# Optimization experiments

Hardware: AMD Instinct MI355X
Metric: run time of the kernel (lower is better)

The kernel has to match this reference:

```python
import jax, jax.numpy as jnp
import numpy as np

N_NODES = 100000
N_EDGES = 3200000
NFEAT = 128
NHID = 128
NCLASS = 8
BN_EPS = 1e-5


def setup_inputs() -> dict:
    key = jax.random.key(0)
    ks = jax.random.split(key, 8)
    x = jax.random.normal(ks[0], (N_NODES, NFEAT), dtype=jnp.float32)
    edge_index = jax.random.randint(ks[1], (2, N_EDGES), 0, N_NODES, dtype=jnp.int64)
    # GCNConv params: weight [nfeat, nhid] (glorot), bias [nhid]
    lim = float(np.sqrt(6.0 / (NFEAT + NHID)))
    W = jax.random.uniform(ks[2], (NFEAT, NHID), minval=-lim, maxval=lim, dtype=jnp.float32)
    b_gc = jnp.zeros((NHID,), dtype=jnp.float32)
    # BatchNorm1d params
    gamma = jnp.ones((NHID,), dtype=jnp.float32)
    beta = jnp.zeros((NHID,), dtype=jnp.float32)
    # fc head: (nhid/2) -> nclass, xavier_uniform, zero bias
    lim2 = float(np.sqrt(6.0 / (NHID // 2 + NCLASS)))
    fc_w = jax.random.uniform(ks[3], (NCLASS, NHID // 2), minval=-lim2, maxval=lim2, dtype=jnp.float32)
    fc_b = jnp.zeros((NCLASS,), dtype=jnp.float32)
    return {"x": x, "edge_index": edge_index, "W": W, "b_gc": b_gc,
            "gamma": gamma, "beta": beta, "fc_w": fc_w, "fc_b": fc_b}


def _gcn_conv(x, edge_index, W, b):
    """PyG GCNConv: add self-loops, symmetric norm, linear, gather-scatter, bias."""
    N = x.shape[0]
    loops = jnp.arange(N, dtype=edge_index.dtype)
    src = jnp.concatenate([edge_index[0], loops])  # source (row / x_j)
    dst = jnp.concatenate([edge_index[1], loops])  # target (col / aggregation index)
    # degree of target nodes (edge weight = 1)
    deg = jax.ops.segment_sum(jnp.ones_like(dst, dtype=x.dtype), dst, num_segments=N)
    dinv = jnp.where(deg > 0, jax.lax.rsqrt(deg), 0.0)
    norm = dinv[src] * dinv[dst]  # [E+N]
    h = x @ W  # [N, nhid]
    msg = h[src] * norm[:, None]  # gather + scale
    out = jax.ops.segment_sum(msg, dst, num_segments=N)  # scatter-add
    return out + b


def _batchnorm(h, gamma, beta):
    mean = jnp.mean(h, axis=0)
    var = jnp.mean(jnp.square(h - mean), axis=0)  # biased, training-mode
    return gamma * (h - mean) * jax.lax.rsqrt(var + BN_EPS) + beta


def reference(x, edge_index, W, b_gc, gamma, beta, fc_w, fc_b):
    h = _gcn_conv(x, edge_index, W, b_gc)
    embed = _batchnorm(h, gamma, beta)
    half = embed.shape[1] // 2
    out = embed[:, :half] @ fc_w.T + fc_b
    return (out, embed)
```

## Files before the change

### kernel.cpp

```cpp
#include <hip/hip_runtime.h>
#include <hip/hip_bf16.h>
#include <math.h>

#define N_NODES 100000
#define N_EDGES 3200000
#define NFEAT 128
#define NHID 128
#define NCLASS 8
#define BN_EPS 1e-5f
#define CB 512
#define NBC 196
#define EPB 8192
#define PART_BLOCKS 391
#define WT_BLOCKS 64

typedef __attribute__((ext_vector_type(8))) short short8;
typedef __attribute__((ext_vector_type(4))) float f32x4;

__device__ __forceinline__ short f2bf(float f) {
    __hip_bfloat16 b = __float2bfloat16(f);
    return *reinterpret_cast<short*>(&b);
}
__device__ __forceinline__ float bf_lo(unsigned u) { return __uint_as_float(u << 16); }
__device__ __forceinline__ float bf_hi(unsigned u) { return __uint_as_float(u & 0xffff0000u); }


__global__ __launch_bounds__(256) void k_chist(const int* __restrict__ dst,
                                               int* __restrict__ ghist,
                                               const float* __restrict__ W,
                                               unsigned short* __restrict__ Wt,
                                               uint4* __restrict__ hbz) {
    if (blockIdx.x >= PART_BLOCKS) {
        int idx = (blockIdx.x - PART_BLOCKS) * 256 + threadIdx.x;
        if (idx < 16) hbz[idx] = (uint4){0u, 0u, 0u, 0u};
        int k = idx >> 7, n = idx & 127;
        Wt[n * NFEAT + k] = (unsigned short)f2bf(W[idx]);
        return;
    }
    __shared__ int lh[NBC];
    const int tid = threadIdx.x;
    if (tid < NBC) lh[tid] = 0;
    __syncthreads();
    const int4* dst4 = (const int4*)dst;
    const int q0 = blockIdx.x * (EPB / 4) + tid;
#pragma unroll
    for (int i = 0; i < 8; ++i) {
        int q = q0 + i * 256;
        if (q < N_EDGES / 4) {
            int4 d = dst4[q];
            atomicAdd(&lh[d.x >> 9], 1);
            atomicAdd(&lh[d.y >> 9], 1);
            atomicAdd(&lh[d.z >> 9], 1);
            atomicAdd(&lh[d.w >> 9], 1);
        }
    }
    __syncthreads();
    if (tid < NBC) {
        int c = lh[tid];
        if (c) atomicAdd(&ghist[tid], c);
    }
}

__global__ __launch_bounds__(512) void k_cscan(const int* __restrict__ ghist,
                                               int* __restrict__ coff,
                                               int* __restrict__ ccur,
                                               int* __restrict__ off,
                                               float* __restrict__ stats,
                                               int* __restrict__ ticket) {
    __shared__ int tmp[512];
    const int t = threadIdx.x;
    if (t < 256) stats[t] = 0.f;
    if (t == 0) *ticket = 0;
    int v = (t < NBC) ? ghist[t] : 0;
    tmp[t] = v;
    __syncthreads();
    for (int d = 1; d < 512; d <<= 1) {
        int u = (t >= d) ? tmp[t - d] : 0;
        __syncthreads();
        tmp[t] += u;
        __syncthreads();
    }
    int excl = tmp[t] - v;
    if (t < NBC) {
        coff[t] = excl;
        ccur[t] = excl;
    }
    if (t == NBC - 1) {
        coff[NBC] = tmp[t];
        off[N_NODES] = tmp[t];
    }
}


__global__ __launch_bounds__(256) void k_part(const int* __restrict__ src,
                                              const int* __restrict__ dst,
                                              int* __restrict__ ccur,
                                              unsigned* __restrict__ epack) {
    __shared__ int lh[NBC];
    __shared__ int lstart[NBC];
    __shared__ int adj[NBC];
    __shared__ int stmp[256];
    __shared__ unsigned sorted[EPB];
    __shared__ unsigned short bkt[EPB];
    const int tid = threadIdx.x;
    if (tid < NBC) lh[tid] = 0;
    __syncthreads();
    const int4* src4 = (const int4*)src;
    const int4* dst4 = (const int4*)dst;
    const int q0 = blockIdx.x * (EPB / 4) + tid;
    int4 sv[8], dv[8];
    int rk[32];
#pragma unroll
    for (int i = 0; i < 8; ++i) {
        int q = q0 + i * 256;
        if (q < N_EDGES / 4) {
            sv[i] = src4[q];
            dv[i] = dst4[q];
            rk[i * 4 + 0] = atomicAdd(&lh[dv[i].x >> 9], 1);
            rk[i * 4 + 1] = atomicAdd(&lh[dv[i].y >> 9], 1);
            rk[i * 4 + 2] = atomicAdd(&lh[dv[i].z >> 9], 1);
            rk[i * 4 + 3] = atomicAdd(&lh[dv[i].w >> 9], 1);
        } else dv[i].x = -1;
    }
    __syncthreads();
    int v = (tid < NBC) ? lh[tid] : 0;
    stmp[tid] = v;
    __syncthreads();
    for (int d = 1; d < 256; d <<= 1) {
        int u = (tid >= d) ? stmp[tid - d] : 0;
        __syncthreads();
        stmp[tid] += u;
        __syncthreads();
    }
    if (tid < NBC) {
        int ls = stmp[tid] - v;
        lstart[tid] = ls;
        adj[tid] = (v ? atomicAdd(&ccur[tid], v) : 0) - ls;
    }
    __syncthreads();
#pragma unroll
    for (int i = 0; i < 8; ++i) {
        if (dv[i].x >= 0) {
            int b, p;
            b = dv[i].x >> 9; p = lstart[b] + rk[i * 4 + 0];
            sorted[p] = ((unsigned)sv[i].x << 9) | (unsigned)(dv[i].x & 511); bkt[p] = (unsigned short)b;
            b = dv[i].y >> 9; p = lstart[b] + rk[i * 4 + 1];
            sorted[p] = ((unsigned)sv[i].y << 9) | (unsigned)(dv[i].y & 511); bkt[p] = (unsigned short)b;
            b = dv[i].z >> 9; p = lstart[b] + rk[i * 4 + 2];
            sorted[p] = ((unsigned)sv[i].z << 9) | (unsigned)(dv[i].z & 511); bkt[p] = (unsigned short)b;
            b = dv[i].w >> 9; p = lstart[b] + rk[i * 4 + 3];
            sorted[p] = ((unsigned)sv[i].w << 9) | (unsigned)(dv[i].w & 511); bkt[p] = (unsigned short)b;
        }
    }
    __syncthreads();
    const int vcnt = stmp[255];
    for (int p = tid; p < vcnt; p += 256)
        epack[p + adj[bkt[p]]] = sorted[p];
}


__global__ __launch_bounds__(256) void k_fine(const unsigned* __restrict__ epack,
                                              const int* __restrict__ coff,
                                              int* __restrict__ off,
                                              float* __restrict__ dinv,
                                              int* __restrict__ esrc) {
    __shared__ int lh[CB], lcur[CB], lsc[256];
    const int tid = threadIdx.x;
    const int b = blockIdx.x;
    const int node0 = b << 9;
    lh[tid] = 0;
    lh[tid + 256] = 0;
    __syncthreads();
    const int lo = coff[b], hiEnd = coff[b + 1];
    for (int i = lo + tid; i < hiEnd; i += 256)
        atomicAdd(&lh[epack[i] & 511u], 1);
    __syncthreads();
    int v0 = lh[2 * tid], v1 = lh[2 * tid + 1];
    int s = v0 + v1;
    lsc[tid] = s;
    __syncthreads();
    for (int d = 1; d < 256; d <<= 1) {
        int u = (tid >= d) ? lsc[tid - d] : 0;
        __syncthreads();
        lsc[tid] += u;
        __syncthreads();
    }
    int pairExcl = lsc[tid] - s;
    lcur[2 * tid] = pairExcl;
    lcur[2 * tid + 1] = pairExcl + v0;
    int n0 = node0 + 2 * tid, n1 = n0 + 1;
    if (n0 < N_NODES) { off[n0] = lo + pairExcl;      dinv[n0] = rsqrtf((float)(v0 + 1)); }
    if (n1 < N_NODES) { off[n1] = lo + pairExcl + v0; dinv[n1] = rsqrtf((float)(v1 + 1)); }
    __syncthreads();
    for (int i = lo + tid; i < hiEnd; i += 256) {
        unsigned p = epack[i];
        int pos = atomicAdd(&lcur[p & 511u], 1);
        esrc[lo + pos] = (int)(p >> 9);
    }
}


#define WSTRIDE 136
#define XSTRIDE 136
__global__ __launch_bounds__(256) void k_gemm(const float* __restrict__ x,
                                              const unsigned short* __restrict__ Wt,
                                              const float* __restrict__ dinv,
                                              unsigned short* __restrict__ hb) {
    __shared__ __align__(16) short wlds[NHID * WSTRIDE];
    __shared__ __align__(16) short xl[64 * XSTRIDE];
    const int tid = threadIdx.x;
    const int row0 = blockIdx.x * 64;

    const unsigned* Wt32 = (const unsigned*)Wt;
    unsigned* wl32 = (unsigned*)wlds;
#pragma unroll
    for (int i = 0; i < 32; ++i) {
        int d = tid + i * 256;
        int n = d >> 6, kp = d & 63;
        wl32[n * (WSTRIDE / 2) + kp] = Wt32[d];
    }
    const float4* x4 = (const float4*)x;
#pragma unroll
    for (int i = 0; i < 8; ++i) {
        int idx = tid + i * 256;
        int r = idx >> 5, c4 = idx & 31;
        int gr = row0 + r;
        float4 vv = (gr < N_NODES) ? x4[(size_t)gr * 32 + c4]
                                   : (float4){0.f, 0.f, 0.f, 0.f};
        short4 t;
        t.x = f2bf(vv.x); t.y = f2bf(vv.y); t.z = f2bf(vv.z); t.w = f2bf(vv.w);
        *(short4*)&xl[r * XSTRIDE + c4 * 4] = t;
    }
    __syncthreads();

    const int wid = tid >> 6, lane = tid & 63;
    const int qw = lane >> 4, lr = lane & 15;

    short8 a[4];
#pragma unroll
    for (int ks = 0; ks < 4; ++ks)
        a[ks] = *(const short8*)&xl[(wid * 16 + lr) * XSTRIDE + ks * 32 + qw * 8];

    f32x4 acc[8];
#pragma unroll
    for (int nt = 0; nt < 8; ++nt) acc[nt] = (f32x4){0.f, 0.f, 0.f, 0.f};

#pragma unroll
    for (int nt = 0; nt < 8; ++nt) {
#pragma unroll
        for (int ks = 0; ks < 4; ++ks) {
            short8 bfr = *(const short8*)&wlds[(nt * 16 + lr) * WSTRIDE + ks * 32 + qw * 8];
            acc[nt] = __builtin_amdgcn_mfma_f32_16x16x32_bf16(a[ks], bfr, acc[nt], 0, 0, 0);
        }
    }

    const int rbase = blockIdx.x * 64 + wid * 16 + qw * 4;
    float dv[4];
#pragma unroll
    for (int j = 0; j < 4; ++j) dv[j] = (rbase + j < N_NODES) ? dinv[rbase + j] : 0.f;
#pragma unroll
    for (int j = 0; j < 4; ++j) {
        int r = rbase + j;
        if (r >= N_NODES) continue;
#pragma unroll
        for (int nt = 0; nt < 8; ++nt)
            hb[(size_t)r * NHID + nt * 16 + lr] = (unsigned short)f2bf(dv[j] * acc[nt][j]);
    }
}


__global__ __launch_bounds__(256) void k_agg(const int* __restrict__ off,
                                             const int* __restrict__ esrc,
                                             const float* __restrict__ dinv,
                                             const uint2* __restrict__ hbq,
                                             float4* __restrict__ agg4) {
    const int node = (blockIdx.x << 2) | (threadIdx.x >> 6);
    const int lane = threadIdx.x & 63;
    const int hl = lane >> 5;
    const int cl = lane & 31;
    if (node >= N_NODES) return;

    const float dn = dinv[node];
    const int self = hl ? N_NODES : node;
    uint2 u0 = hbq[(size_t)self * 32 + cl];
    float aAx = bf_lo(u0.x), aAy = bf_hi(u0.x), aAz = bf_lo(u0.y), aAw = bf_hi(u0.y);
    float aBx = 0.f, aBy = 0.f, aBz = 0.f, aBw = 0.f;
    float aCx = 0.f, aCy = 0.f, aCz = 0.f, aCw = 0.f;
    float aDx = 0.f, aDy = 0.f, aDz = 0.f, aDw = 0.f;

    const int begin = off[node], end = off[node + 1];
    for (int base = begin; base < end; base += 64) {
        int m = end - base;
        if (m > 64) m = 64;
        int sv = (lane < m) ? esrc[base + lane] : N_NODES;
        const int kmax = (m + 7) >> 3;
        for (int k = 0; k < kmax; ++k) {
            int sA = __shfl(sv, 8 * k + 0 + hl);
            int sB = __shfl(sv, 8 * k + 2 + hl);
            int sC = __shfl(sv, 8 * k + 4 + hl);
            int sD = __shfl(sv, 8 * k + 6 + hl);
            uint2 uA = hbq[(size_t)sA * 32 + cl];
            uint2 uB = hbq[(size_t)sB * 32 + cl];
            uint2 uC = hbq[(size_t)sC * 32 + cl];
            uint2 uD = hbq[(size_t)sD * 32 + cl];
            aAx += bf_lo(uA.x); aAy += bf_hi(uA.x); aAz += bf_lo(uA.y); aAw += bf_hi(uA.y);
            aBx += bf_lo(uB.x); aBy += bf_hi(uB.x); aBz += bf_lo(uB.y); aBw += bf_hi(uB.y);
            aCx += bf_lo(uC.x); aCy += bf_hi(uC.x); aCz += bf_lo(uC.y); aCw += bf_hi(uC.y);
            aDx += bf_lo(uD.x); aDy += bf_hi(uD.x); aDz += bf_lo(uD.y); aDw += bf_hi(uD.y);
        }
    }
    float ax = (aAx + aBx) + (aCx + aDx);
    float ay = (aAy + aBy) + (aCy + aDy);
    float az = (aAz + aBz) + (aCz + aDz);
    float aw = (aAw + aBw) + (aCw + aDw);
    ax += __shfl_xor(ax, 32);
    ay += __shfl_xor(ay, 32);
    az += __shfl_xor(az, 32);
    aw += __shfl_xor(aw, 32);
    if (hl == 0) {
        float4 o;
        o.x = ax * dn; o.y = ay * dn; o.z = az * dn; o.w = aw * dn;
        agg4[(size_t)node * 32 + cl] = o;
    }
}


__global__ __launch_bounds__(256) void k_stats(const float* __restrict__ agg,
                                               float* __restrict__ stats,
                                               int* __restrict__ ticket,
                                               const float* __restrict__ gamma,
                                               const float* __restrict__ beta,
                                               float* __restrict__ ss) {
    const int cb = threadIdx.x & 31;
    const int rg = threadIdx.x >> 5;
    const float4* a4 = (const float4*)agg;
    float4 s = {0.f, 0.f, 0.f, 0.f}, s2 = {0.f, 0.f, 0.f, 0.f};
    for (int r = blockIdx.x * 8 + rg; r < N_NODES; r += gridDim.x * 8) {
        float4 v = a4[(size_t)r * 32 + cb];
        s.x += v.x; s.y += v.y; s.z += v.z; s.w += v.w;
        s2.x += v.x * v.x; s2.y += v.y * v.y; s2.z += v.z * v.z; s2.w += v.w * v.w;
    }
    __shared__ float4 ls[256], ls2[256];
    __shared__ int lastflag;
    ls[threadIdx.x] = s;
    ls2[threadIdx.x] = s2;
    __syncthreads();
    if (rg == 0) {
        float4 ts = ls[cb], t2 = ls2[cb];
#pragma unroll
        for (int g = 1; g < 8; ++g) {
            float4 v = ls[g * 32 + cb], w = ls2[g * 32 + cb];
            ts.x += v.x; ts.y += v.y; ts.z += v.z; ts.w += v.w;
            t2.x += w.x; t2.y += w.y; t2.z += w.z; t2.w += w.w;
        }
        atomicAdd(&stats[cb * 4 + 0], ts.x);
        atomicAdd(&stats[cb * 4 + 1], ts.y);
        atomicAdd(&stats[cb * 4 + 2], ts.z);
        atomicAdd(&stats[cb * 4 + 3], ts.w);
        atomicAdd(&stats[128 + cb * 4 + 0], t2.x);
        atomicAdd(&stats[128 + cb * 4 + 1], t2.y);
        atomicAdd(&stats[128 + cb * 4 + 2], t2.z);
        atomicAdd(&stats[128 + cb * 4 + 3], t2.w);
    }
    __threadfence();
    __syncthreads();
    if (threadIdx.x == 0)
        lastflag = (atomicAdd(ticket, 1) == (int)gridDim.x - 1) ? 1 : 0;
    __syncthreads();
    if (lastflag && threadIdx.x < NHID) {
        int c = threadIdx.x;
        float sum = atomicAdd(&stats[c], 0.f);
        float sq  = atomicAdd(&stats[128 + c], 0.f);
        float mean = sum / (float)N_NODES;
        float var = fmaxf(sq / (float)N_NODES - mean * mean, 0.f);
        float inv = rsqrtf(var + BN_EPS);
        float sc = gamma[c] * inv;
        ss[c] = sc;
        ss[128 + c] = beta[c] - mean * sc;
    }
}


__global__ __launch_bounds__(256) void k_bnfc(float* __restrict__ embed,
                                              const float* __restrict__ ss,
                                              const float* __restrict__ fc_w,
                                              const float* __restrict__ fc_b,
                                              float* __restrict__ out) {
    __shared__ float se[64][68];
    __shared__ float sw[8][68];
    __shared__ float sb[8];
    const int tid = threadIdx.x;
    const int row0 = blockIdx.x * 64;
    {
        int d = tid;
        sw[d >> 6][d & 63] = fc_w[d];
        d = tid + 256;
        sw[d >> 6][d & 63] = fc_w[d];
        if (tid < 8) sb[tid] = fc_b[tid];
    }
    float4* ef4 = (float4*)embed;
    const float4* ssc4 = (const float4*)ss;
    const float4* ssh4 = (const float4*)(ss + 128);
#pragma unroll
    for (int i = 0; i < 8; ++i) {
        int d = tid + i * 256;
        int r = d >> 5;
        int cb = d & 31;
        int gr = row0 + r;
        if (gr < N_NODES) {
            float4 v = ef4[(size_t)gr * 32 + cb];
            float4 sc = ssc4[cb], sh = ssh4[cb];
            v.x = fmaf(v.x, sc.x, sh.x);
            v.y = fmaf(v.y, sc.y, sh.y);
            v.z = fmaf(v.z, sc.z, sh.z);
            v.w = fmaf(v.w, sc.w, sh.w);
            ef4[(size_t)gr * 32 + cb] = v;
            if (cb < 16) {
                se[r][cb * 4 + 0] = v.x; se[r][cb * 4 + 1] = v.y;
                se[r][cb * 4 + 2] = v.z; se[r][cb * 4 + 3] = v.w;
            }
        } else if (cb < 16) {
            se[r][cb * 4 + 0] = 0.f; se[r][cb * 4 + 1] = 0.f;
            se[r][cb * 4 + 2] = 0.f; se[r][cb * 4 + 3] = 0.f;
        }
    }
    __syncthreads();
    const int r = tid >> 2;
    const int j0 = (tid & 3) * 2;
    const int gr = row0 + r;
#pragma unroll
    for (int jj = 0; jj < 2; ++jj) {
        int j = j0 + jj;
        float s = sb[j];
#pragma unroll
        for (int k = 0; k < 64; ++k) s = fmaf(se[r][k], sw[j][k], s);
        if (gr < N_NODES) out[(size_t)gr * NCLASS + j] = s;
    }
}


extern "C" void kernel_launch(void* const* d_in, const int* in_sizes, int n_in,
                              void* d_out, int out_size, void* d_ws, size_t ws_size,
                              hipStream_t stream) {
    const float* x     = (const float*)d_in[0];
    const int*   ei    = (const int*)d_in[1];
    const float* W     = (const float*)d_in[2];
    const float* gamma = (const float*)d_in[4];
    const float* beta  = (const float*)d_in[5];
    const float* fc_w  = (const float*)d_in[6];
    const float* fc_b  = (const float*)d_in[7];

    const int* src = ei;
    const int* dst = ei + N_EDGES;

    float* out   = (float*)d_out;
    float* embed = (float*)d_out + (size_t)N_NODES * NCLASS;

    char* ws = (char*)d_ws;
    size_t o = 0;
    unsigned* epack = (unsigned*)(ws + o);          o += (size_t)N_EDGES * 4;
    unsigned short* hb = (unsigned short*)(ws + o); o += (size_t)(N_NODES + 1) * NHID * 2;
    o = (o + 255) & ~(size_t)255;
    int* esrc   = (int*)(ws + o);                   o += (size_t)N_EDGES * 4;
    int* off    = (int*)(ws + o);                   o += (size_t)(N_NODES + 1) * 4;
    float* dinv = (float*)(ws + o);                 o += (size_t)N_NODES * 4;
    unsigned short* Wt = (unsigned short*)(ws + o); o += (size_t)NFEAT * NHID * 2;
    float* stats = (float*)(ws + o);                o += 256 * 4;
    float* ss    = (float*)(ws + o);                o += 256 * 4;
    int* ghist   = (int*)(ws + o);                  o += NBC * 4;
    int* coff    = (int*)(ws + o);                  o += (NBC + 1) * 4;
    int* ccur    = (int*)(ws + o);                  o += NBC * 4;
    int* ticket  = (int*)(ws + o);                  o += 4;

    hipMemsetAsync(ghist, 0, NBC * 4, stream);

    k_chist<<<PART_BLOCKS + WT_BLOCKS, 256, 0, stream>>>(dst, ghist, W, Wt,
                                                         (uint4*)(hb + (size_t)N_NODES * NHID));
    k_cscan<<<1, 512, 0, stream>>>(ghist, coff, ccur, off, stats, ticket);
    k_part<<<PART_BLOCKS, 256, 0, stream>>>(src, dst, ccur, epack);
    k_fine<<<NBC, 256, 0, stream>>>(epack, coff, off, dinv, esrc);

    k_gemm<<<(N_NODES + 63) / 64, 256, 0, stream>>>(x, Wt, dinv, hb);

    k_agg<<<(N_NODES + 3) / 4, 256, 0, stream>>>(off, esrc, dinv, (const uint2*)hb, (float4*)embed);

    k_stats<<<512, 256, 0, stream>>>(embed, stats, ticket, gamma, beta, ss);

    k_bnfc<<<(N_NODES + 63) / 64, 256, 0, stream>>>(embed, ss, fc_w, fc_b, out);
}
```

Measured before the change: 319.7 us.

## Fuse BN stats and BN+FC into one kernel with a grid-wide flag barrier

Merges the stats and BN/FC kernels into one persistent 512-block kernel. The last block to finish the stats computes the scale and shift, then sets a flag that the other blocks spin on before running the BN+FC tiles. This saves a launch and may reuse cached embed data. The histogram now writes per-block partials instead of using a memset and global atomics, the W transpose moves into the single-block scan kernel, and the bucket array shrinks to bytes. The spin barrier is only safe if all 512 blocks are co-resident. The serial 391-iteration reduction and the 16K-element transpose in a single block may also add latency.

```diff
diff --git a/kernel.cpp b/kernel.cpp
--- a/kernel.cpp
+++ b/kernel.cpp
@@ -12,7 +12,8 @@
 #define NBC 196
 #define EPB 8192
 #define PART_BLOCKS 391
-#define WT_BLOCKS 64
+#define NT_BNFC 1563
+#define SB_BLOCKS 512
 
 typedef __attribute__((ext_vector_type(8))) short short8;
 typedef __attribute__((ext_vector_type(4))) float f32x4;
@@ -26,17 +27,7 @@
 
 
 __global__ __launch_bounds__(256) void k_chist(const int* __restrict__ dst,
-                                               int* __restrict__ ghist,
-                                               const float* __restrict__ W,
-                                               unsigned short* __restrict__ Wt,
-                                               uint4* __restrict__ hbz) {
-    if (blockIdx.x >= PART_BLOCKS) {
-        int idx = (blockIdx.x - PART_BLOCKS) * 256 + threadIdx.x;
-        if (idx < 16) hbz[idx] = (uint4){0u, 0u, 0u, 0u};
-        int k = idx >> 7, n = idx & 127;
-        Wt[n * NFEAT + k] = (unsigned short)f2bf(W[idx]);
-        return;
-    }
+                                               int* __restrict__ ghist2) {
     __shared__ int lh[NBC];
     const int tid = threadIdx.x;
     if (tid < NBC) lh[tid] = 0;
@@ -55,23 +46,34 @@
         }
     }
     __syncthreads();
-    if (tid < NBC) {
-        int c = lh[tid];
-        if (c) atomicAdd(&ghist[tid], c);
-    }
-}
-
-__global__ __launch_bounds__(512) void k_cscan(const int* __restrict__ ghist,
+    if (tid < NBC) ghist2[blockIdx.x * NBC + tid] = lh[tid];
+}
+
+
+__global__ __launch_bounds__(512) void k_cscan(const int* __restrict__ ghist2,
                                                int* __restrict__ coff,
                                                int* __restrict__ ccur,
                                                int* __restrict__ off,
                                                float* __restrict__ stats,
-                                               int* __restrict__ ticket) {
+                                               int* __restrict__ ticket,
+                                               int* __restrict__ flag,
+                                               const float* __restrict__ W,
+                                               unsigned short* __restrict__ Wt,
+                                               unsigned short* __restrict__ hbzrow) {
     __shared__ int tmp[512];
     const int t = threadIdx.x;
     if (t < 256) stats[t] = 0.f;
-    if (t == 0) *ticket = 0;
-    int v = (t < NBC) ? ghist[t] : 0;
+    if (t == 0) { *ticket = 0; *flag = 0; }
+    if (t < NHID) hbzrow[t] = 0;
+#pragma unroll
+    for (int i = 0; i < 32; ++i) {
+        int idx = t + i * 512;
+        int k = idx >> 7, n = idx & 127;
+        Wt[n * NFEAT + k] = (unsigned short)f2bf(W[idx]);
+    }
+    int v = 0;
+    if (t < NBC)
+        for (int b = 0; b < PART_BLOCKS; ++b) v += ghist2[b * NBC + t];
     tmp[t] = v;
     __syncthreads();
     for (int d = 1; d < 512; d <<= 1) {
@@ -101,7 +103,7 @@
     __shared__ int adj[NBC];
     __shared__ int stmp[256];
     __shared__ unsigned sorted[EPB];
-    __shared__ unsigned short bkt[EPB];
+    __shared__ unsigned char bkt[EPB];
     const int tid = threadIdx.x;
     if (tid < NBC) lh[tid] = 0;
     __syncthreads();
@@ -143,13 +145,13 @@
         if (dv[i].x >= 0) {
             int b, p;
             b = dv[i].x >> 9; p = lstart[b] + rk[i * 4 + 0];
-            sorted[p] = ((unsigned)sv[i].x << 9) | (unsigned)(dv[i].x & 511); bkt[p] = (unsigned short)b;
+            sorted[p] = ((unsigned)sv[i].x << 9) | (unsigned)(dv[i].x & 511); bkt[p] = (unsigned char)b;
             b = dv[i].y >> 9; p = lstart[b] + rk[i * 4 + 1];
-            sorted[p] = ((unsigned)sv[i].y << 9) | (unsigned)(dv[i].y & 511); bkt[p] = (unsigned short)b;
+            sorted[p] = ((unsigned)sv[i].y << 9) | (unsigned)(dv[i].y & 511); bkt[p] = (unsigned char)b;
             b = dv[i].z >> 9; p = lstart[b] + rk[i * 4 + 2];
-            sorted[p] = ((unsigned)sv[i].z << 9) | (unsigned)(dv[i].z & 511); bkt[p] = (unsigned short)b;
+            sorted[p] = ((unsigned)sv[i].z << 9) | (unsigned)(dv[i].z & 511); bkt[p] = (unsigned char)b;
             b = dv[i].w >> 9; p = lstart[b] + rk[i * 4 + 3];
-            sorted[p] = ((unsigned)sv[i].w << 9) | (unsigned)(dv[i].w & 511); bkt[p] = (unsigned short)b;
+            sorted[p] = ((unsigned)sv[i].w << 9) | (unsigned)(dv[i].w & 511); bkt[p] = (unsigned char)b;
         }
     }
     __syncthreads();
@@ -325,116 +327,129 @@
 }
 
 
-__global__ __launch_bounds__(256) void k_stats(const float* __restrict__ agg,
-                                               float* __restrict__ stats,
-                                               int* __restrict__ ticket,
-                                               const float* __restrict__ gamma,
-                                               const float* __restrict__ beta,
-                                               float* __restrict__ ss) {
-    const int cb = threadIdx.x & 31;
-    const int rg = threadIdx.x >> 5;
-    const float4* a4 = (const float4*)agg;
-    float4 s = {0.f, 0.f, 0.f, 0.f}, s2 = {0.f, 0.f, 0.f, 0.f};
-    for (int r = blockIdx.x * 8 + rg; r < N_NODES; r += gridDim.x * 8) {
-        float4 v = a4[(size_t)r * 32 + cb];
-        s.x += v.x; s.y += v.y; s.z += v.z; s.w += v.w;
-        s2.x += v.x * v.x; s2.y += v.y * v.y; s2.z += v.z * v.z; s2.w += v.w * v.w;
-    }
-    __shared__ float4 ls[256], ls2[256];
+__global__ __launch_bounds__(256) void k_statsbnfc(float* __restrict__ embed,
+                                                   float* __restrict__ stats,
+                                                   int* __restrict__ ticket,
+                                                   int* __restrict__ flag,
+                                                   const float* __restrict__ gamma,
+                                                   const float* __restrict__ beta,
+                                                   float* __restrict__ ss,
+                                                   const float* __restrict__ fc_w,
+                                                   const float* __restrict__ fc_b,
+                                                   float* __restrict__ out) {
+    const int tid = threadIdx.x;
+    {
+        const int cb = tid & 31;
+        const int rg = tid >> 5;
+        const float4* a4 = (const float4*)embed;
+        float4 s = {0.f, 0.f, 0.f, 0.f}, s2 = {0.f, 0.f, 0.f, 0.f};
+        for (int r = blockIdx.x * 8 + rg; r < N_NODES; r += SB_BLOCKS * 8) {
+            float4 v = a4[(size_t)r * 32 + cb];
+            s.x += v.x; s.y += v.y; s.z += v.z; s.w += v.w;
+            s2.x += v.x * v.x; s2.y += v.y * v.y; s2.z += v.z * v.z; s2.w += v.w * v.w;
+        }
+        __shared__ float4 ls[256], ls2[256];
+        ls[tid] = s;
+        ls2[tid] = s2;
+        __syncthreads();
+        if (rg == 0) {
+            float4 ts = ls[cb], t2 = ls2[cb];
+#pragma unroll
+            for (int g = 1; g < 8; ++g) {
+                float4 v = ls[g * 32 + cb], w = ls2[g * 32 + cb];
+                ts.x += v.x; ts.y += v.y; ts.z += v.z; ts.w += v.w;
+                t2.x += w.x; t2.y += w.y; t2.z += w.z; t2.w += w.w;
+            }
+            atomicAdd(&stats[cb * 4 + 0], ts.x);
+            atomicAdd(&stats[cb * 4 + 1], ts.y);
+            atomicAdd(&stats[cb * 4 + 2], ts.z);
+            atomicAdd(&stats[cb * 4 + 3], ts.w);
+            atomicAdd(&stats[128 + cb * 4 + 0], t2.x);
+            atomicAdd(&stats[128 + cb * 4 + 1], t2.y);
+            atomicAdd(&stats[128 + cb * 4 + 2], t2.z);
+            atomicAdd(&stats[128 + cb * 4 + 3], t2.w);
+        }
+    }
+    __threadfence();
+    __syncthreads();
     __shared__ int lastflag;
-    ls[threadIdx.x] = s;
-    ls2[threadIdx.x] = s2;
-    __syncthreads();
-    if (rg == 0) {
-        float4 ts = ls[cb], t2 = ls2[cb];
-#pragma unroll
-        for (int g = 1; g < 8; ++g) {
-            float4 v = ls[g * 32 + cb], w = ls2[g * 32 + cb];
-            ts.x += v.x; ts.y += v.y; ts.z += v.z; ts.w += v.w;
-            t2.x += w.x; t2.y += w.y; t2.z += w.z; t2.w += w.w;
-        }
-        atomicAdd(&stats[cb * 4 + 0], ts.x);
-        atomicAdd(&stats[cb * 4 + 1], ts.y);
-        atomicAdd(&stats[cb * 4 + 2], ts.z);
-        atomicAdd(&stats[cb * 4 + 3], ts.w);
-        atomicAdd(&stats[128 + cb * 4 + 0], t2.x);
-        atomicAdd(&stats[128 + cb * 4 + 1], t2.y);
-        atomicAdd(&stats[128 + cb * 4 + 2], t2.z);
-        atomicAdd(&stats[128 + cb * 4 + 3], t2.w);
-    }
-    __threadfence();
-    __syncthreads();
-    if (threadIdx.x == 0)
-        lastflag = (atomicAdd(ticket, 1) == (int)gridDim.x - 1) ? 1 : 0;
-    __syncthreads();
-    if (lastflag && threadIdx.x < NHID) {
-        int c = threadIdx.x;
-        float sum = atomicAdd(&stats[c], 0.f);
-        float sq  = atomicAdd(&stats[128 + c], 0.f);
-        float mean = sum / (float)N_NODES;
-        float var = fmaxf(sq / (float)N_NODES - mean * mean, 0.f);
-        float inv = rsqrtf(var + BN_EPS);
-        float sc = gamma[c] * inv;
-        ss[c] = sc;
-        ss[128 + c] = beta[c] - mean * sc;
-    }
-}
-
-
-__global__ __launch_bounds__(256) void k_bnfc(float* __restrict__ embed,
-                                              const float* __restrict__ ss,
-                                              const float* __restrict__ fc_w,
-                                              const float* __restrict__ fc_b,
-                                              float* __restrict__ out) {
+    if (tid == 0)
+        lastflag = (atomicAdd(ticket, 1) == SB_BLOCKS - 1) ? 1 : 0;
+    __syncthreads();
+    if (lastflag) {
+        if (tid < NHID) {
+            int c = tid;
+            float sum = atomicAdd(&stats[c], 0.f);
+            float sq  = atomicAdd(&stats[128 + c], 0.f);
+            float mean = sum / (float)N_NODES;
+            float var = fmaxf(sq / (float)N_NODES - mean * mean, 0.f);
+            float inv = rsqrtf(var + BN_EPS);
+            float sc = gamma[c] * inv;
+            ss[c] = sc;
+            ss[128 + c] = beta[c] - mean * sc;
+        }
+        __syncthreads();
+        if (tid == 0) {
+            __threadfence();
+            atomicExch(flag, 1);
+        }
+    } else {
+        if (tid == 0)
+            while (atomicAdd(flag, 0) == 0) { }
+        __syncthreads();
+        __threadfence();
+    }
     __shared__ float se[64][68];
     __shared__ float sw[8][68];
     __shared__ float sb[8];
-    const int tid = threadIdx.x;
-    const int row0 = blockIdx.x * 64;
     {
         int d = tid;
-        sw[d >> 6][d & 63] = fc_w[d];
+        if (d < 512) sw[d >> 6][d & 63] = fc_w[d];
         d = tid + 256;
-        sw[d >> 6][d & 63] = fc_w[d];
+        if (d < 512) sw[d >> 6][d & 63] = fc_w[d];
         if (tid < 8) sb[tid] = fc_b[tid];
     }
     float4* ef4 = (float4*)embed;
     const float4* ssc4 = (const float4*)ss;
     const float4* ssh4 = (const float4*)(ss + 128);
-#pragma unroll
-    for (int i = 0; i < 8; ++i) {
-        int d = tid + i * 256;
-        int r = d >> 5;
-        int cb = d & 31;
-        int gr = row0 + r;
-        if (gr < N_NODES) {
-            float4 v = ef4[(size_t)gr * 32 + cb];
-            float4 sc = ssc4[cb], sh = ssh4[cb];
-            v.x = fmaf(v.x, sc.x, sh.x);
-            v.y = fmaf(v.y, sc.y, sh.y);
-            v.z = fmaf(v.z, sc.z, sh.z);
-            v.w = fmaf(v.w, sc.w, sh.w);
-            ef4[(size_t)gr * 32 + cb] = v;
-            if (cb < 16) {
-                se[r][cb * 4 + 0] = v.x; se[r][cb * 4 + 1] = v.y;
-                se[r][cb * 4 + 2] = v.z; se[r][cb * 4 + 3] = v.w;
+    for (int tile = blockIdx.x; tile < NT_BNFC; tile += SB_BLOCKS) {
+        const int row0 = tile * 64;
+        __syncthreads();
+#pragma unroll
+        for (int i = 0; i < 8; ++i) {
+            int d = tid + i * 256;
+            int r = d >> 5;
+            int cb = d & 31;
+            int gr = row0 + r;
+            if (gr < N_NODES) {
+                float4 v = ef4[(size_t)gr * 32 + cb];
+                float4 sc = ssc4[cb], sh = ssh4[cb];
+                v.x = fmaf(v.x, sc.x, sh.x);
+                v.y = fmaf(v.y, sc.y, sh.y);
+                v.z = fmaf(v.z, sc.z, sh.z);
+                v.w = fmaf(v.w, sc.w, sh.w);
+                ef4[(size_t)gr * 32 + cb] = v;
+                if (cb < 16) {
+                    se[r][cb * 4 + 0] = v.x; se[r][cb * 4 + 1] = v.y;
+                    se[r][cb * 4 + 2] = v.z; se[r][cb * 4 + 3] = v.w;
+                }
+            } else if (cb < 16) {
+                se[r][cb * 4 + 0] = 0.f; se[r][cb * 4 + 1] = 0.f;
+                se[r][cb * 4 + 2] = 0.f; se[r][cb * 4 + 3] = 0.f;
             }
-        } else if (cb < 16) {
-            se[r][cb * 4 + 0] = 0.f; se[r][cb * 4 + 1] = 0.f;
-            se[r][cb * 4 + 2] = 0.f; se[r][cb * 4 + 3] = 0.f;
-        }
-    }
-    __syncthreads();
-    const int r = tid >> 2;
-    const int j0 = (tid & 3) * 2;
-    const int gr = row0 + r;
-#pragma unroll
-    for (int jj = 0; jj < 2; ++jj) {
-        int j = j0 + jj;
-        float s = sb[j];
-#pragma unroll
-        for (int k = 0; k < 64; ++k) s = fmaf(se[r][k], sw[j][k], s);
-        if (gr < N_NODES) out[(size_t)gr * NCLASS + j] = s;
+        }
+        __syncthreads();
+        const int r = tid >> 2;
+        const int j0 = (tid & 3) * 2;
+        const int gr = row0 + r;
+#pragma unroll
+        for (int jj = 0; jj < 2; ++jj) {
+            int j = j0 + jj;
+            float s = sb[j];
+#pragma unroll
+            for (int k = 0; k < 64; ++k) s = fmaf(se[r][k], sw[j][k], s);
+            if (gr < N_NODES) out[(size_t)gr * NCLASS + j] = s;
+        }
     }
 }
 
@@ -465,18 +480,18 @@
     int* off    = (int*)(ws + o);                   o += (size_t)(N_NODES + 1) * 4;
     float* dinv = (float*)(ws + o);                 o += (size_t)N_NODES * 4;
     unsigned short* Wt = (unsigned short*)(ws + o); o += (size_t)NFEAT * NHID * 2;
+    o = (o + 15) & ~(size_t)15;
     float* stats = (float*)(ws + o);                o += 256 * 4;
     float* ss    = (float*)(ws + o);                o += 256 * 4;
-    int* ghist   = (int*)(ws + o);                  o += NBC * 4;
+    int* ghist2  = (int*)(ws + o);                  o += (size_t)PART_BLOCKS * NBC * 4;
     int* coff    = (int*)(ws + o);                  o += (NBC + 1) * 4;
     int* ccur    = (int*)(ws + o);                  o += NBC * 4;
     int* ticket  = (int*)(ws + o);                  o += 4;
-
-    hipMemsetAsync(ghist, 0, NBC * 4, stream);
-
-    k_chist<<<PART_BLOCKS + WT_BLOCKS, 256, 0, stream>>>(dst, ghist, W, Wt,
-                                                         (uint4*)(hb + (size_t)N_NODES * NHID));
-    k_cscan<<<1, 512, 0, stream>>>(ghist, coff, ccur, off, stats, ticket);
+    int* flag    = (int*)(ws + o);                  o += 4;
+
+    k_chist<<<PART_BLOCKS, 256, 0, stream>>>(dst, ghist2);
+    k_cscan<<<1, 512, 0, stream>>>(ghist2, coff, ccur, off, stats, ticket, flag,
+                                   W, Wt, hb + (size_t)N_NODES * NHID);
     k_part<<<PART_BLOCKS, 256, 0, stream>>>(src, dst, ccur, epack);
     k_fine<<<NBC, 256, 0, stream>>>(epack, coff, off, dinv, esrc);
 
@@ -484,7 +499,6 @@
 
     k_agg<<<(N_NODES + 3) / 4, 256, 0, stream>>>(off, esrc, dinv, (const uint2*)hb, (float4*)embed);
 
-    k_stats<<<512, 256, 0, stream>>>(embed, stats, ticket, gamma, beta, ss);
-
-    k_bnfc<<<(N_NODES + 63) / 64, 256, 0, stream>>>(embed, ss, fc_w, fc_b, out);
-}
+    k_statsbnfc<<<SB_BLOCKS, 256, 0, stream>>>(embed, stats, ticket, flag,
+                                               gamma, beta, ss, fc_w, fc_b, out);
+}
```

New measurement: 386.9 us. +21.0%, slower.

## Fuse GEMM with dst histogram and move source-degree scaling into aggregation

Applied to the files above, without the earlier changes.

The x@W GEMM no longer depends on dinv. It is merged into the first launch alongside the destination histogram blocks, and each GEMM block converts W to bf16 in LDS itself. The source-side dinv scaling moves into the aggregation kernel: each lane loads dinv[src] alongside the edge index, shuffles it, and uses FMAs. This removes one launch and the Wt staging, and lets the GEMM run concurrently with histogram work. In exchange the aggregation does an extra gather per edge, every GEMM block re-converts W redundantly, and the bucket array shrinks to bytes.

```diff
diff --git a/kernel.cpp b/kernel.cpp
--- a/kernel.cpp
+++ b/kernel.cpp
@@ -12,7 +12,7 @@
 #define NBC 196
 #define EPB 8192
 #define PART_BLOCKS 391
-#define WT_BLOCKS 64
+#define GEMM_BLOCKS 1563
 
 typedef __attribute__((ext_vector_type(8))) short short8;
 typedef __attribute__((ext_vector_type(4))) float f32x4;
@@ -25,52 +25,110 @@
 __device__ __forceinline__ float bf_hi(unsigned u) { return __uint_as_float(u & 0xffff0000u); }
 
 
-__global__ __launch_bounds__(256) void k_chist(const int* __restrict__ dst,
-                                               int* __restrict__ ghist,
-                                               const float* __restrict__ W,
-                                               unsigned short* __restrict__ Wt,
-                                               uint4* __restrict__ hbz) {
-    if (blockIdx.x >= PART_BLOCKS) {
-        int idx = (blockIdx.x - PART_BLOCKS) * 256 + threadIdx.x;
-        if (idx < 16) hbz[idx] = (uint4){0u, 0u, 0u, 0u};
+#define WSTRIDE 136
+#define XSTRIDE 136
+__global__ __launch_bounds__(256) void k_prep(const float* __restrict__ x,
+                                              const float* __restrict__ W,
+                                              unsigned short* __restrict__ hb,
+                                              const int* __restrict__ dst,
+                                              int* __restrict__ ghist) {
+    __shared__ __align__(16) short wlds[NHID * WSTRIDE];
+    __shared__ __align__(16) short xl[64 * XSTRIDE];
+    const int tid = threadIdx.x;
+
+    if (blockIdx.x >= GEMM_BLOCKS) {
+        __shared__ int lh[NBC];
+        if (tid < NBC) lh[tid] = 0;
+        __syncthreads();
+        const int4* dst4 = (const int4*)dst;
+        const int q0 = (blockIdx.x - GEMM_BLOCKS) * (EPB / 4) + tid;
+#pragma unroll
+        for (int i = 0; i < 8; ++i) {
+            int q = q0 + i * 256;
+            if (q < N_EDGES / 4) {
+                int4 d = dst4[q];
+                atomicAdd(&lh[d.x >> 9], 1);
+                atomicAdd(&lh[d.y >> 9], 1);
+                atomicAdd(&lh[d.z >> 9], 1);
+                atomicAdd(&lh[d.w >> 9], 1);
+            }
+        }
+        __syncthreads();
+        if (tid < NBC) {
+            int c = lh[tid];
+            if (c) atomicAdd(&ghist[tid], c);
+        }
+        return;
+    }
+
+    const int row0 = blockIdx.x * 64;
+
+#pragma unroll 8
+    for (int i = 0; i < 64; ++i) {
+        int idx = tid + i * 256;
         int k = idx >> 7, n = idx & 127;
-        Wt[n * NFEAT + k] = (unsigned short)f2bf(W[idx]);
-        return;
-    }
-    __shared__ int lh[NBC];
-    const int tid = threadIdx.x;
-    if (tid < NBC) lh[tid] = 0;
-    __syncthreads();
-    const int4* dst4 = (const int4*)dst;
-    const int q0 = blockIdx.x * (EPB / 4) + tid;
+        wlds[n * WSTRIDE + k] = f2bf(W[idx]);
+    }
+    const float4* x4 = (const float4*)x;
 #pragma unroll
     for (int i = 0; i < 8; ++i) {
-        int q = q0 + i * 256;
-        if (q < N_EDGES / 4) {
-            int4 d = dst4[q];
-            atomicAdd(&lh[d.x >> 9], 1);
-            atomicAdd(&lh[d.y >> 9], 1);
-            atomicAdd(&lh[d.z >> 9], 1);
-            atomicAdd(&lh[d.w >> 9], 1);
-        }
-    }
-    __syncthreads();
-    if (tid < NBC) {
-        int c = lh[tid];
-        if (c) atomicAdd(&ghist[tid], c);
-    }
-}
+        int idx = tid + i * 256;
+        int r = idx >> 5, c4 = idx & 31;
+        int gr = row0 + r;
+        float4 vv = (gr < N_NODES) ? x4[(size_t)gr * 32 + c4]
+                                   : (float4){0.f, 0.f, 0.f, 0.f};
+        short4 t;
+        t.x = f2bf(vv.x); t.y = f2bf(vv.y); t.z = f2bf(vv.z); t.w = f2bf(vv.w);
+        *(short4*)&xl[r * XSTRIDE + c4 * 4] = t;
+    }
+    __syncthreads();
+
+    const int wid = tid >> 6, lane = tid & 63;
+    const int qw = lane >> 4, lr = lane & 15;
+
+    short8 a[4];
+#pragma unroll
+    for (int ks = 0; ks < 4; ++ks)
+        a[ks] = *(const short8*)&xl[(wid * 16 + lr) * XSTRIDE + ks * 32 + qw * 8];
+
+    f32x4 acc[8];
+#pragma unroll
+    for (int nt = 0; nt < 8; ++nt) acc[nt] = (f32x4){0.f, 0.f, 0.f, 0.f};
+
+#pragma unroll
+    for (int nt = 0; nt < 8; ++nt) {
+#pragma unroll
+        for (int ks = 0; ks < 4; ++ks) {
+            short8 bfr = *(const short8*)&wlds[(nt * 16 + lr) * WSTRIDE + ks * 32 + qw * 8];
+            acc[nt] = __builtin_amdgcn_mfma_f32_16x16x32_bf16(a[ks], bfr, acc[nt], 0, 0, 0);
+        }
+    }
+
+    const int rbase = row0 + wid * 16 + qw * 4;
+#pragma unroll
+    for (int j = 0; j < 4; ++j) {
+        int r = rbase + j;
+        if (r >= N_NODES) continue;
+#pragma unroll
+        for (int nt = 0; nt < 8; ++nt)
+            hb[(size_t)r * NHID + nt * 16 + lr] = (unsigned short)f2bf(acc[nt][j]);
+    }
+}
+
 
 __global__ __launch_bounds__(512) void k_cscan(const int* __restrict__ ghist,
                                                int* __restrict__ coff,
                                                int* __restrict__ ccur,
                                                int* __restrict__ off,
                                                float* __restrict__ stats,
-                                               int* __restrict__ ticket) {
+                                               int* __restrict__ ticket,
+                                               unsigned short* __restrict__ hbzrow,
+                                               float* __restrict__ dinv) {
     __shared__ int tmp[512];
     const int t = threadIdx.x;
     if (t < 256) stats[t] = 0.f;
-    if (t == 0) *ticket = 0;
+    if (t == 0) { *ticket = 0; dinv[N_NODES] = 0.f; }
+    if (t < NHID) hbzrow[t] = 0;
     int v = (t < NBC) ? ghist[t] : 0;
     tmp[t] = v;
     __syncthreads();
@@ -101,7 +159,7 @@
     __shared__ int adj[NBC];
     __shared__ int stmp[256];
     __shared__ unsigned sorted[EPB];
-    __shared__ unsigned short bkt[EPB];
+    __shared__ unsigned char bkt[EPB];
     const int tid = threadIdx.x;
     if (tid < NBC) lh[tid] = 0;
     __syncthreads();
@@ -143,13 +201,13 @@
         if (dv[i].x >= 0) {
             int b, p;
             b = dv[i].x >> 9; p = lstart[b] + rk[i * 4 + 0];
-            sorted[p] = ((unsigned)sv[i].x << 9) | (unsigned)(dv[i].x & 511); bkt[p] = (unsigned short)b;
+            sorted[p] = ((unsigned)sv[i].x << 9) | (unsigned)(dv[i].x & 511); bkt[p] = (unsigned char)b;
             b = dv[i].y >> 9; p = lstart[b] + rk[i * 4 + 1];
-            sorted[p] = ((unsigned)sv[i].y << 9) | (unsigned)(dv[i].y & 511); bkt[p] = (unsigned short)b;
+            sorted[p] = ((unsigned)sv[i].y << 9) | (unsigned)(dv[i].y & 511); bkt[p] = (unsigned char)b;
             b = dv[i].z >> 9; p = lstart[b] + rk[i * 4 + 2];
-            sorted[p] = ((unsigned)sv[i].z << 9) | (unsigned)(dv[i].z & 511); bkt[p] = (unsigned short)b;
+            sorted[p] = ((unsigned)sv[i].z << 9) | (unsigned)(dv[i].z & 511); bkt[p] = (unsigned char)b;
             b = dv[i].w >> 9; p = lstart[b] + rk[i * 4 + 3];
-            sorted[p] = ((unsigned)sv[i].w << 9) | (unsigned)(dv[i].w & 511); bkt[p] = (unsigned short)b;
+            sorted[p] = ((unsigned)sv[i].w << 9) | (unsigned)(dv[i].w & 511); bkt[p] = (unsigned char)b;
         }
     }
     __syncthreads();
@@ -200,75 +258,6 @@
 }
 
 
-#define WSTRIDE 136
-#define XSTRIDE 136
-__global__ __launch_bounds__(256) void k_gemm(const float* __restrict__ x,
-                                              const unsigned short* __restrict__ Wt,
-                                              const float* __restrict__ dinv,
-                                              unsigned short* __restrict__ hb) {
-    __shared__ __align__(16) short wlds[NHID * WSTRIDE];
-    __shared__ __align__(16) short xl[64 * XSTRIDE];
-    const int tid = threadIdx.x;
-    const int row0 = blockIdx.x * 64;
-
-    const unsigned* Wt32 = (const unsigned*)Wt;
-    unsigned* wl32 = (unsigned*)wlds;
-#pragma unroll
-    for (int i = 0; i < 32; ++i) {
-        int d = tid + i * 256;
-        int n = d >> 6, kp = d & 63;
-        wl32[n * (WSTRIDE / 2) + kp] = Wt32[d];
-    }
-    const float4* x4 = (const float4*)x;
-#pragma unroll
-    for (int i = 0; i < 8; ++i) {
-        int idx = tid + i * 256;
-        int r = idx >> 5, c4 = idx & 31;
-        int gr = row0 + r;
-        float4 vv = (gr < N_NODES) ? x4[(size_t)gr * 32 + c4]
-                                   : (float4){0.f, 0.f, 0.f, 0.f};
-        short4 t;
-        t.x = f2bf(vv.x); t.y = f2bf(vv.y); t.z = f2bf(vv.z); t.w = f2bf(vv.w);
-        *(short4*)&xl[r * XSTRIDE + c4 * 4] = t;
-    }
-    __syncthreads();
-
-    const int wid = tid >> 6, lane = tid & 63;
-    const int qw = lane >> 4, lr = lane & 15;
-
-    short8 a[4];
-#pragma unroll
-    for (int ks = 0; ks < 4; ++ks)
-        a[ks] = *(const short8*)&xl[(wid * 16 + lr) * XSTRIDE + ks * 32 + qw * 8];
-
-    f32x4 acc[8];
-#pragma unroll
-    for (int nt = 0; nt < 8; ++nt) acc[nt] = (f32x4){0.f, 0.f, 0.f, 0.f};
-
-#pragma unroll
-    for (int nt = 0; nt < 8; ++nt) {
-#pragma unroll
-        for (int ks = 0; ks < 4; ++ks) {
-            short8 bfr = *(const short8*)&wlds[(nt * 16 + lr) * WSTRIDE + ks * 32 + qw * 8];
-            acc[nt] = __builtin_amdgcn_mfma_f32_16x16x32_bf16(a[ks], bfr, acc[nt], 0, 0, 0);
-        }
-    }
-
-    const int rbase = blockIdx.x * 64 + wid * 16 + qw * 4;
-    float dv[4];
-#pragma unroll
-    for (int j = 0; j < 4; ++j) dv[j] = (rbase + j < N_NODES) ? dinv[rbase + j] : 0.f;
-#pragma unroll
-    for (int j = 0; j < 4; ++j) {
-        int r = rbase + j;
-        if (r >= N_NODES) continue;
-#pragma unroll
-        for (int nt = 0; nt < 8; ++nt)
-            hb[(size_t)r * NHID + nt * 16 + lr] = (unsigned short)f2bf(dv[j] * acc[nt][j]);
-    }
-}
-
-
 __global__ __launch_bounds__(256) void k_agg(const int* __restrict__ off,
                                              const int* __restrict__ esrc,
                                              const float* __restrict__ dinv,
@@ -283,7 +272,8 @@
     const float dn = dinv[node];
     const int self = hl ? N_NODES : node;
     uint2 u0 = hbq[(size_t)self * 32 + cl];
-    float aAx = bf_lo(u0.x), aAy = bf_hi(u0.x), aAz = bf_lo(u0.y), aAw = bf_hi(u0.y);
+    float aAx = dn * bf_lo(u0.x), aAy = dn * bf_hi(u0.x);
+    float aAz = dn * bf_lo(u0.y), aAw = dn * bf_hi(u0.y);
     float aBx = 0.f, aBy = 0.f, aBz = 0.f, aBw = 0.f;
     float aCx = 0.f, aCy = 0.f, aCz = 0.f, aCw = 0.f;
     float aDx = 0.f, aDy = 0.f, aDz = 0.f, aDw = 0.f;
@@ -292,21 +282,34 @@
     for (int base = begin; base < end; base += 64) {
         int m = end - base;
         if (m > 64) m = 64;
-        int sv = (lane < m) ? esrc[base + lane] : N_NODES;
+        int sv = N_NODES;
+        float dw = 0.f;
+        if (lane < m) {
+            sv = esrc[base + lane];
+            dw = dinv[sv];
+        }
         const int kmax = (m + 7) >> 3;
         for (int k = 0; k < kmax; ++k) {
             int sA = __shfl(sv, 8 * k + 0 + hl);
             int sB = __shfl(sv, 8 * k + 2 + hl);
             int sC = __shfl(sv, 8 * k + 4 + hl);
             int sD = __shfl(sv, 8 * k + 6 + hl);
+            float wA = __shfl(dw, 8 * k + 0 + hl);
+            float wB = __shfl(dw, 8 * k + 2 + hl);
+            float wC = __shfl(dw, 8 * k + 4 + hl);
+            float wD = __shfl(dw, 8 * k + 6 + hl);
             uint2 uA = hbq[(size_t)sA * 32 + cl];
             uint2 uB = hbq[(size_t)sB * 32 + cl];
             uint2 uC = hbq[(size_t)sC * 32 + cl];
             uint2 uD = hbq[(size_t)sD * 32 + cl];
-            aAx += bf_lo(uA.x); aAy += bf_hi(uA.x); aAz += bf_lo(uA.y); aAw += bf_hi(uA.y);
-            aBx += bf_lo(uB.x); aBy += bf_hi(uB.x); aBz += bf_lo(uB.y); aBw += bf_hi(uB.y);
-            aCx += bf_lo(uC.x); aCy += bf_hi(uC.x); aCz += bf_lo(uC.y); aCw += bf_hi(uC.y);
-            aDx += bf_lo(uD.x); aDy += bf_hi(uD.x); aDz += bf_lo(uD.y); aDw += bf_hi(uD.y);
+            aAx = fmaf(wA, bf_lo(uA.x), aAx); aAy = fmaf(wA, bf_hi(uA.x), aAy);
+            aAz = fmaf(wA, bf_lo(uA.y), aAz); aAw = fmaf(wA, bf_hi(uA.y), aAw);
+            aBx = fmaf(wB, bf_lo(uB.x), aBx); aBy = fmaf(wB, bf_hi(uB.x), aBy);
+            aBz = fmaf(wB, bf_lo(uB.y), aBz); aBw = fmaf(wB, bf_hi(uB.y), aBw);
+            aCx = fmaf(wC, bf_lo(uC.x), aCx); aCy = fmaf(wC, bf_hi(uC.x), aCy);
+            aCz = fmaf(wC, bf_lo(uC.y), aCz); aCw = fmaf(wC, bf_hi(uC.y), aCw);
+            aDx = fmaf(wD, bf_lo(uD.x), aDx); aDy = fmaf(wD, bf_hi(uD.x), aDy);
+            aDz = fmaf(wD, bf_lo(uD.y), aDz); aDw = fmaf(wD, bf_hi(uD.y), aDw);
         }
     }
     float ax = (aAx + aBx) + (aCx + aDx);
@@ -463,8 +466,7 @@
     o = (o + 255) & ~(size_t)255;
     int* esrc   = (int*)(ws + o);                   o += (size_t)N_EDGES * 4;
     int* off    = (int*)(ws + o);                   o += (size_t)(N_NODES + 1) * 4;
-    float* dinv = (float*)(ws + o);                 o += (size_t)N_NODES * 4;
-    unsigned short* Wt = (unsigned short*)(ws + o); o += (size_t)NFEAT * NHID * 2;
+    float* dinv = (float*)(ws + o);                 o += (size_t)(N_NODES + 1) * 4;
     float* stats = (float*)(ws + o);                o += 256 * 4;
     float* ss    = (float*)(ws + o);                o += 256 * 4;
     int* ghist   = (int*)(ws + o);                  o += NBC * 4;
@@ -474,14 +476,13 @@
 
     hipMemsetAsync(ghist, 0, NBC * 4, stream);
 
-    k_chist<<<PART_BLOCKS + WT_BLOCKS, 256, 0, stream>>>(dst, ghist, W, Wt,
-                                                         (uint4*)(hb + (size_t)N_NODES * NHID));
-    k_cscan<<<1, 512, 0, stream>>>(ghist, coff, ccur, off, stats, ticket);
+    k_prep<<<GEMM_BLOCKS + PART_BLOCKS, 256, 0, stream>>>(x, W, hb, dst, ghist);
+
+    k_cscan<<<1, 512, 0, stream>>>(ghist, coff, ccur, off, stats, ticket,
+                                   hb + (size_t)N_NODES * NHID, dinv);
     k_part<<<PART_BLOCKS, 256, 0, stream>>>(src, dst, ccur, epack);
     k_fine<<<NBC, 256, 0, stream>>>(epack, coff, off, dinv, esrc);
 
-    k_gemm<<<(N_NODES + 63) / 64, 256, 0, stream>>>(x, Wt, dinv, hb);
-
     k_agg<<<(N_NODES + 3) / 4, 256, 0, stream>>>(off, esrc, dinv, (const uint2*)hb, (float4*)embed);
 
     k_stats<<<512, 256, 0, stream>>>(embed, stats, ticket, gamma, beta, ss);
```

New measurement: 320.7 us. Within noise of the previous version (+0.3%).
